# Optimization experiments

Measured on AMD Instinct MI355X. Metric: run time of the kernel, lower is better.

## Reference

```python
import jax, jax.numpy as jnp
import numpy as np

NUM_GROUPS = 256   # number of distinct gt instance ids per image
EPS = 1e-6
PULL_W = 1.0
PUSH_W = 1.0
LOSS_W = 1.0


def setup_inputs() -> dict:
    key = jax.random.key(0)
    k1, k2, k3 = jax.random.split(key, 3)
    B, N, D = 16, 16384, 256
    pred = jax.random.normal(k1, (B, N, D), dtype=jnp.float32)
    gt_inds = jax.random.randint(k2, (B, N), 0, NUM_GROUPS, dtype=jnp.int32)
    anchor_inds = jax.random.randint(k3, (B, N), 0, 9, dtype=jnp.int32)
    return {"pred": pred, "gt_inds": gt_inds, "anchor_inds": anchor_inds}


def _single_image_loss(p, g):
    # p: [N, D] tag embeddings, g: [N] int group ids in [0, NUM_GROUPS)
    ones = jnp.ones(g.shape, dtype=p.dtype)
    counts = jax.ops.segment_sum(ones, g, num_segments=NUM_GROUPS)          # [G]
    sums = jax.ops.segment_sum(p, g, num_segments=NUM_GROUPS)               # [G, D]
    tags = sums / jnp.maximum(counts, 1.0)[:, None]                         # group means

    # pull: per-element cosine to own group's tag (torch cos eps clamp on norm product)
    tag_per = tags[g]                                                       # [N, D]
    dot = jnp.sum(p * tag_per, axis=1)
    denom = jnp.maximum(jnp.linalg.norm(p, axis=1) * jnp.linalg.norm(tag_per, axis=1), EPS)
    one_minus_cos = 1.0 - dot / denom                                       # [N]
    pull_g = jax.ops.segment_sum(one_minus_cos, g, num_segments=NUM_GROUPS) / jnp.maximum(counts, 1.0)

    present = counts > 0
    obj_num = jnp.sum(present.astype(p.dtype))
    pull = jnp.sum(jnp.where(present, pull_g, 0.0)) / (obj_num + EPS)

    # push: pairwise cosine over group tags (incl. diagonal, then subtract 2*obj_num)
    tn = jnp.linalg.norm(tags, axis=1)                                      # [G]
    cosmat = (tags @ tags.T) / jnp.maximum(tn[:, None] * tn[None, :], EPS)  # [G, G]
    pair_mask = present[:, None] & present[None, :]
    push_sum = jnp.sum(jnp.where(pair_mask, 1.0 + cosmat, 0.0)) - 2.0 * obj_num
    push = push_sum / (((obj_num - 1.0) * obj_num + EPS) * 2.0)

    loss = PUSH_W * push + PULL_W * pull
    # original returns 0 when only a single group exists
    return jnp.where(obj_num > 1.0, loss, 0.0)


def reference(pred, gt_inds, anchor_inds):
    per_img = jax.vmap(_single_image_loss)(pred, gt_inds)   # [B]
    return LOSS_W * jnp.mean(per_img)
```

## Files before the change

### kernel.cpp

```cpp
#include <hip/hip_runtime.h>

#define B_ 16
#define N_ 16384
#define D_ 256
#define G_ 256
#define EPSF 1e-6f

template <int CTRL>
__device__ __forceinline__ float dpp_add_step(float x) {
    const int y = __builtin_amdgcn_update_dpp(0, __float_as_int(x), CTRL, 0xF, 0xF, false);
    return x + __int_as_float(y);
}
__device__ __forceinline__ float wave_sum64(float x) {
    x = dpp_add_step<0x111>(x);
    x = dpp_add_step<0x112>(x);
    x = dpp_add_step<0x114>(x);
    x = dpp_add_step<0x118>(x);
    x = dpp_add_step<0x142>(x);
    x = dpp_add_step<0x143>(x);
    return __int_as_float(__builtin_amdgcn_readlane(__float_as_int(x), 63));
}

__global__ __launch_bounds__(1024) void k_sort(const int* __restrict__ gt,
                                               int* __restrict__ counts,
                                               int* __restrict__ starts,
                                               int* __restrict__ sorted,
                                               int* __restrict__ done) {
    __shared__ int hist[G_];
    __shared__ int scn[G_];
    const int tid = threadIdx.x, b = blockIdx.x;
    if (b == 0 && tid == 0) done[0] = 0;
    if (tid < G_) hist[tid] = 0;
    __syncthreads();
    const int base = b * N_;
    #pragma unroll
    for (int k = 0; k < N_/4096; ++k) {
        const int4 g4 = *(const int4*)&gt[base + k*4096 + tid*4];
        atomicAdd(&hist[g4.x], 1);
        atomicAdd(&hist[g4.y], 1);
        atomicAdd(&hist[g4.z], 1);
        atomicAdd(&hist[g4.w], 1);
    }
    __syncthreads();
    int c = 0;
    if (tid < G_) {
        c = hist[tid];
        counts[b*G_ + tid] = c;
        scn[tid] = c;
    }
    __syncthreads();
    for (int off = 1; off < G_; off <<= 1) {
        int v = 0;
        if (tid < G_ && tid >= off) v = scn[tid - off];
        __syncthreads();
        if (tid < G_) scn[tid] += v;
        __syncthreads();
    }
    if (tid < G_) {
        const int st = scn[tid] - c;
        starts[b*G_ + tid] = st;
        hist[tid] = st;
    }
    __syncthreads();
    #pragma unroll
    for (int k = 0; k < N_/4096; ++k) {
        const int r = k*4096 + tid*4;
        const int4 g4 = *(const int4*)&gt[base + r];
        sorted[base + atomicAdd(&hist[g4.x], 1)] = r;
        sorted[base + atomicAdd(&hist[g4.y], 1)] = r + 1;
        sorted[base + atomicAdd(&hist[g4.z], 1)] = r + 2;
        sorted[base + atomicAdd(&hist[g4.w], 1)] = r + 3;
    }
}

__global__ __launch_bounds__(256, 5) void k_fused(const float* __restrict__ pred,
                                                  const int* __restrict__ sorted,
                                                  const int* __restrict__ starts,
                                                  const int* __restrict__ counts,
                                                  float* __restrict__ sums,
                                                  float* __restrict__ pull_g) {
    __shared__ float comb[2][2][2][D_];
    const int tid = threadIdx.x, lane = tid & 63, w = tid >> 6;
    const int sub = w >> 1, h = w & 1;
    const int gi = (blockIdx.x << 1) | sub;
    const int b = gi >> 8;
    const int start = starts[gi], cnt = counts[gi];
    const int c = lane * 4;

    const float* predb = pred + (size_t)b*N_*D_;
    const int*   sortb = sorted + b*N_ + start;

    float4 acc  = make_float4(0.f,0.f,0.f,0.f);
    float4 uacc = make_float4(0.f,0.f,0.f,0.f);

    const int half = (cnt + 1) >> 1;
    const int lo = h * half;
    const int hi = min(cnt, lo + half);
    int i = lo;

    if (cnt > 0 && cnt <= 128) {
        const int ids0 = sortb[min(lane, cnt-1)];
        int ids1 = 0;
        if (cnt > 64) ids1 = sortb[min(64 + lane, cnt-1)];
        #define GET2(k) (((k) < 64) ? __builtin_amdgcn_readlane(ids0, (k)) \
                                    : __builtin_amdgcn_readlane(ids1, (k) - 64))
        for (; i + 8 <= hi; i += 8) {
            const int r0 = GET2(i+0), r1 = GET2(i+1), r2 = GET2(i+2), r3 = GET2(i+3);
            const int r4 = GET2(i+4), r5 = GET2(i+5), r6 = GET2(i+6), r7 = GET2(i+7);
            const float4 p0 = *(const float4*)&predb[(size_t)r0*D_ + c];
            const float4 p1 = *(const float4*)&predb[(size_t)r1*D_ + c];
            const float4 p2 = *(const float4*)&predb[(size_t)r2*D_ + c];
            const float4 p3 = *(const float4*)&predb[(size_t)r3*D_ + c];
            const float4 p4 = *(const float4*)&predb[(size_t)r4*D_ + c];
            const float4 p5 = *(const float4*)&predb[(size_t)r5*D_ + c];
            const float4 p6 = *(const float4*)&predb[(size_t)r6*D_ + c];
            const float4 p7 = *(const float4*)&predb[(size_t)r7*D_ + c];
            float n0 = p0.x*p0.x + p0.y*p0.y + p0.z*p0.z + p0.w*p0.w;
            float n1 = p1.x*p1.x + p1.y*p1.y + p1.z*p1.z + p1.w*p1.w;
            float n2 = p2.x*p2.x + p2.y*p2.y + p2.z*p2.z + p2.w*p2.w;
            float n3 = p3.x*p3.x + p3.y*p3.y + p3.z*p3.z + p3.w*p3.w;
            float n4 = p4.x*p4.x + p4.y*p4.y + p4.z*p4.z + p4.w*p4.w;
            float n5 = p5.x*p5.x + p5.y*p5.y + p5.z*p5.z + p5.w*p5.w;
            float n6 = p6.x*p6.x + p6.y*p6.y + p6.z*p6.z + p6.w*p6.w;
            float n7 = p7.x*p7.x + p7.y*p7.y + p7.z*p7.z + p7.w*p7.w;
            n0 = wave_sum64(n0); n1 = wave_sum64(n1);
            n2 = wave_sum64(n2); n3 = wave_sum64(n3);
            n4 = wave_sum64(n4); n5 = wave_sum64(n5);
            n6 = wave_sum64(n6); n7 = wave_sum64(n7);
            const float q0 = __frsqrt_rn(n0), q1 = __frsqrt_rn(n1);
            const float q2 = __frsqrt_rn(n2), q3 = __frsqrt_rn(n3);
            const float q4 = __frsqrt_rn(n4), q5 = __frsqrt_rn(n5);
            const float q6 = __frsqrt_rn(n6), q7 = __frsqrt_rn(n7);
            acc.x  += ((p0.x + p1.x) + (p2.x + p3.x)) + ((p4.x + p5.x) + (p6.x + p7.x));
            acc.y  += ((p0.y + p1.y) + (p2.y + p3.y)) + ((p4.y + p5.y) + (p6.y + p7.y));
            acc.z  += ((p0.z + p1.z) + (p2.z + p3.z)) + ((p4.z + p5.z) + (p6.z + p7.z));
            acc.w  += ((p0.w + p1.w) + (p2.w + p3.w)) + ((p4.w + p5.w) + (p6.w + p7.w));
            uacc.x += ((p0.x*q0 + p1.x*q1) + (p2.x*q2 + p3.x*q3)) + ((p4.x*q4 + p5.x*q5) + (p6.x*q6 + p7.x*q7));
            uacc.y += ((p0.y*q0 + p1.y*q1) + (p2.y*q2 + p3.y*q3)) + ((p4.y*q4 + p5.y*q5) + (p6.y*q6 + p7.y*q7));
            uacc.z += ((p0.z*q0 + p1.z*q1) + (p2.z*q2 + p3.z*q3)) + ((p4.z*q4 + p5.z*q5) + (p6.z*q6 + p7.z*q7));
            uacc.w += ((p0.w*q0 + p1.w*q1) + (p2.w*q2 + p3.w*q3)) + ((p4.w*q4 + p5.w*q5) + (p6.w*q6 + p7.w*q7));
        }
        for (; i < hi; ++i) {
            const int r0 = GET2(i);
            const float4 p0 = *(const float4*)&predb[(size_t)r0*D_ + c];
            const float n0 = wave_sum64(p0.x*p0.x + p0.y*p0.y + p0.z*p0.z + p0.w*p0.w);
            const float q0 = __frsqrt_rn(n0);
            acc.x  += p0.x;    acc.y  += p0.y;    acc.z  += p0.z;    acc.w  += p0.w;
            uacc.x += p0.x*q0; uacc.y += p0.y*q0; uacc.z += p0.z*q0; uacc.w += p0.w*q0;
        }
        #undef GET2
    } else if (cnt > 128) {
        for (; i < hi; ++i) {
            const int r0 = sortb[i];
            const float4 p0 = *(const float4*)&predb[(size_t)r0*D_ + c];
            const float n0 = wave_sum64(p0.x*p0.x + p0.y*p0.y + p0.z*p0.z + p0.w*p0.w);
            const float q0 = __frsqrt_rn(n0);
            acc.x  += p0.x;    acc.y  += p0.y;    acc.z  += p0.z;    acc.w  += p0.w;
            uacc.x += p0.x*q0; uacc.y += p0.y*q0; uacc.z += p0.z*q0; uacc.w += p0.w*q0;
        }
    }

    *(float4*)&comb[sub][h][0][c] = acc;
    *(float4*)&comb[sub][h][1][c] = uacc;
    __syncthreads();
    if (h != 0) return;

    const float4 a2 = *(const float4*)&comb[sub][1][0][c];
    const float4 u2 = *(const float4*)&comb[sub][1][1][c];
    acc.x  += a2.x;  acc.y  += a2.y;  acc.z  += a2.z;  acc.w  += a2.w;
    uacc.x += u2.x;  uacc.y += u2.y;  uacc.z += u2.z;  uacc.w += u2.w;

    *(float4*)&sums[(size_t)gi*D_ + c] = acc;
    if (cnt == 0) {
        if (lane == 0) pull_g[gi] = 0.f;
        return;
    }
    const float ssq = wave_sum64(acc.x*acc.x + acc.y*acc.y + acc.z*acc.z + acc.w*acc.w);
    const float dus = wave_sum64(uacc.x*acc.x + uacc.y*acc.y + uacc.z*acc.z + uacc.w*acc.w);
    if (lane == 0) pull_g[gi] = (float)cnt - dus / sqrtf(ssq);
}

__global__ __launch_bounds__(256) void k_tags(const float* __restrict__ sums,
                                              const int* __restrict__ counts,
                                              const float* __restrict__ pull_g,
                                              float* __restrict__ lossv,
                                              int* __restrict__ done,
                                              float* __restrict__ out) {
    const int b = blockIdx.x;
    const int tid = threadIdx.x;
    const int lane = tid & 63;
    const int wave = tid >> 6;
    __shared__ float s_acc[D_];
    __shared__ float redA[256];
    __shared__ float redB[256];

    for (int i = tid; i < D_; i += 256) s_acc[i] = 0.f;
    __syncthreads();

    const int c = lane * 4;
    float4 sl = make_float4(0.f, 0.f, 0.f, 0.f);
    for (int g = wave; g < G_; g += 4) {
        const int cnt = counts[b*G_ + g];
        const float inv = 1.0f / fmaxf((float)cnt, 1.0f);
        const float4 sm = *(const float4*)&sums[((size_t)(b*G_ + g))*D_ + c];
        const float tx = sm.x*inv, tyv = sm.y*inv, tz = sm.z*inv, tw = sm.w*inv;
        const float sq = wave_sum64(tx*tx + tyv*tyv + tz*tz + tw*tw);
        if (cnt > 0) {
            const float it = __frsqrt_rn(sq);
            sl.x += tx*it; sl.y += tyv*it; sl.z += tz*it; sl.w += tw*it;
        }
    }
    atomicAdd(&s_acc[c+0], sl.x);
    atomicAdd(&s_acc[c+1], sl.y);
    atomicAdd(&s_acc[c+2], sl.z);
    atomicAdd(&s_acc[c+3], sl.w);
    __syncthreads();

    const int cnt_t = counts[b*G_ + tid];
    const float v = s_acc[tid];
    redA[tid] = v * v;
    redB[tid] = (cnt_t > 0) ? 1.f : 0.f;
    __syncthreads();
    for (int s = 128; s > 0; s >>= 1) {
        if (tid < s) { redA[tid] += redA[tid + s]; redB[tid] += redB[tid + s]; }
        __syncthreads();
    }
    float ssq = 0.f, obj = 0.f;
    if (tid == 0) { ssq = redA[0]; obj = redB[0]; }
    __syncthreads();

    redA[tid] = (cnt_t > 0) ? pull_g[b*G_ + tid] / (float)cnt_t : 0.f;
    __syncthreads();
    for (int s = 128; s > 0; s >>= 1) {
        if (tid < s) redA[tid] += redA[tid + s];
        __syncthreads();
    }
    if (tid == 0) {
        const float push = (obj*obj - 2.f*obj + ssq) / (((obj - 1.f)*obj + EPSF) * 2.f);
        const float pull = redA[0] / (obj + EPSF);
        const float loss = (obj > 1.f) ? (push + pull) : 0.f;
        __hip_atomic_store(&lossv[b], loss, __ATOMIC_RELEASE, __HIP_MEMORY_SCOPE_AGENT);
        const int o = __hip_atomic_fetch_add(&done[0], 1, __ATOMIC_ACQ_REL,
                                             __HIP_MEMORY_SCOPE_AGENT);
        if (o == B_ - 1) {
            float t = 0.f;
            #pragma unroll
            for (int bb = 0; bb < B_; ++bb)
                t += __hip_atomic_load(&lossv[bb], __ATOMIC_RELAXED, __HIP_MEMORY_SCOPE_AGENT);
            out[0] = t * (1.0f / (float)B_);
        }
    }
}

extern "C" void kernel_launch(void* const* d_in, const int* in_sizes, int n_in,
                              void* d_out, int out_size, void* d_ws, size_t ws_size,
                              hipStream_t stream) {
    const float* pred = (const float*)d_in[0];
    const int*   gt   = (const int*)d_in[1];
    float* out = (float*)d_out;

    char* ws = (char*)d_ws;
    const size_t SZ_SUMS = (size_t)B_*G_*D_*sizeof(float);
    const size_t SZ_I    = (size_t)B_*G_*sizeof(int);

    float* sums    = (float*)ws;                               ws += SZ_SUMS;
    int*   counts  = (int*)ws;                                 ws += SZ_I;
    int*   starts  = (int*)ws;                                 ws += SZ_I;
    float* pull_g  = (float*)ws;                               ws += SZ_I;
    float* lossv   = (float*)ws;                               ws += 64*sizeof(float);
    int*   done    = (int*)ws;                                 ws += 64*sizeof(int);
    int*   sorted  = (int*)ws;

    k_sort  <<<B_,      1024, 0, stream>>>(gt, counts, starts, sorted, done);
    k_fused <<<B_*G_/2,  256, 0, stream>>>(pred, sorted, starts, counts, sums, pull_g);
    k_tags  <<<B_,       256, 0, stream>>>(sums, counts, pull_g, lossv, done, out);
}
```

Measured before the change: 90.74 us.

## Split per-image counting sort into chunked histogram and scatter kernels

Replaces the single-block-per-image counting sort (16 blocks) with two kernels over 256 blocks: a per-chunk histogram, then a kernel that computes per-chunk prefix offsets and the global scan and scatters indices. The aim is to spread the sort across more CUs instead of 16. In exchange it adds an extra kernel launch, a global round trip for the chunk histograms, and redundant scans in every block.

```diff
diff --git a/kernel.cpp b/kernel.cpp
--- a/kernel.cpp
+++ b/kernel.cpp
@@ -5,6 +5,8 @@
 #define D_ 256
 #define G_ 256
 #define EPSF 1e-6f
+#define CHUNKS 16
+#define CROWS (N_/CHUNKS)
 
 template <int CTRL>
 __device__ __forceinline__ float dpp_add_step(float x) {
@@ -21,56 +23,61 @@
     return __int_as_float(__builtin_amdgcn_readlane(__float_as_int(x), 63));
 }
 
-__global__ __launch_bounds__(1024) void k_sort(const int* __restrict__ gt,
-                                               int* __restrict__ counts,
-                                               int* __restrict__ starts,
-                                               int* __restrict__ sorted,
-                                               int* __restrict__ done) {
-    __shared__ int hist[G_];
+__global__ __launch_bounds__(256) void k_hist(const int* __restrict__ gt,
+                                              int* __restrict__ chist,
+                                              int* __restrict__ done) {
+    __shared__ int h[G_];
+    const int tid = threadIdx.x, blk = blockIdx.x;
+    if (blk == 0 && tid == 0) done[0] = 0;
+    h[tid] = 0;
+    __syncthreads();
+    const int4 g4 = *(const int4*)&gt[blk*CROWS + tid*4];
+    atomicAdd(&h[g4.x], 1);
+    atomicAdd(&h[g4.y], 1);
+    atomicAdd(&h[g4.z], 1);
+    atomicAdd(&h[g4.w], 1);
+    __syncthreads();
+    chist[blk*G_ + tid] = h[tid];
+}
+
+__global__ __launch_bounds__(256) void k_scatscan(const int* __restrict__ gt,
+                                                  const int* __restrict__ chist,
+                                                  int* __restrict__ counts,
+                                                  int* __restrict__ starts,
+                                                  int* __restrict__ sorted) {
     __shared__ int scn[G_];
-    const int tid = threadIdx.x, b = blockIdx.x;
-    if (b == 0 && tid == 0) done[0] = 0;
-    if (tid < G_) hist[tid] = 0;
-    __syncthreads();
-    const int base = b * N_;
+    __shared__ int cur[G_];
+    const int g = threadIdx.x, blk = blockIdx.x;
+    const int b = blk >> 4, chunk = blk & 15;
+
+    int tot = 0, pre = 0;
     #pragma unroll
-    for (int k = 0; k < N_/4096; ++k) {
-        const int4 g4 = *(const int4*)&gt[base + k*4096 + tid*4];
-        atomicAdd(&hist[g4.x], 1);
-        atomicAdd(&hist[g4.y], 1);
-        atomicAdd(&hist[g4.z], 1);
-        atomicAdd(&hist[g4.w], 1);
-    }
-    __syncthreads();
-    int c = 0;
-    if (tid < G_) {
-        c = hist[tid];
-        counts[b*G_ + tid] = c;
-        scn[tid] = c;
-    }
+    for (int cc = 0; cc < CHUNKS; ++cc) {
+        const int v = chist[((b<<4) + cc)*G_ + g];
+        pre += (cc < chunk) ? v : 0;
+        tot += v;
+    }
+    scn[g] = tot;
     __syncthreads();
     for (int off = 1; off < G_; off <<= 1) {
-        int v = 0;
-        if (tid < G_ && tid >= off) v = scn[tid - off];
-        __syncthreads();
-        if (tid < G_) scn[tid] += v;
-        __syncthreads();
-    }
-    if (tid < G_) {
-        const int st = scn[tid] - c;
-        starts[b*G_ + tid] = st;
-        hist[tid] = st;
-    }
-    __syncthreads();
-    #pragma unroll
-    for (int k = 0; k < N_/4096; ++k) {
-        const int r = k*4096 + tid*4;
-        const int4 g4 = *(const int4*)&gt[base + r];
-        sorted[base + atomicAdd(&hist[g4.x], 1)] = r;
-        sorted[base + atomicAdd(&hist[g4.y], 1)] = r + 1;
-        sorted[base + atomicAdd(&hist[g4.z], 1)] = r + 2;
-        sorted[base + atomicAdd(&hist[g4.w], 1)] = r + 3;
-    }
+        const int v2 = (g >= off) ? scn[g - off] : 0;
+        __syncthreads();
+        scn[g] += v2;
+        __syncthreads();
+    }
+    const int st = scn[g] - tot;
+    if (chunk == 0) { counts[b*G_ + g] = tot; starts[b*G_ + g] = st; }
+    cur[g] = st + pre;
+    __syncthreads();
+
+    const int rbase = chunk * CROWS;
+    const int4 g4 = *(const int4*)&gt[b*N_ + rbase + g*4];
+    const int r = rbase + g*4;
+    int* sb = sorted + b*N_;
+    sb[atomicAdd(&cur[g4.x], 1)] = r;
+    sb[atomicAdd(&cur[g4.y], 1)] = r + 1;
+    sb[atomicAdd(&cur[g4.z], 1)] = r + 2;
+    sb[atomicAdd(&cur[g4.w], 1)] = r + 3;
 }
 
 __global__ __launch_bounds__(256, 5) void k_fused(const float* __restrict__ pred,
@@ -269,9 +276,11 @@
     float* pull_g  = (float*)ws;                               ws += SZ_I;
     float* lossv   = (float*)ws;                               ws += 64*sizeof(float);
     int*   done    = (int*)ws;                                 ws += 64*sizeof(int);
-    int*   sorted  = (int*)ws;
-
-    k_sort  <<<B_,      1024, 0, stream>>>(gt, counts, starts, sorted, done);
-    k_fused <<<B_*G_/2,  256, 0, stream>>>(pred, sorted, starts, counts, sums, pull_g);
-    k_tags  <<<B_,       256, 0, stream>>>(sums, counts, pull_g, lossv, done, out);
-}
+    int*   sorted  = (int*)ws;                                 ws += (size_t)B_*N_*sizeof(int);
+    int*   chist   = (int*)ws;
+
+    k_hist     <<<B_*CHUNKS, 256, 0, stream>>>(gt, chist, done);
+    k_scatscan <<<B_*CHUNKS, 256, 0, stream>>>(gt, chist, counts, starts, sorted);
+    k_fused    <<<B_*G_/2,   256, 0, stream>>>(pred, sorted, starts, counts, sums, pull_g);
+    k_tags     <<<B_,        256, 0, stream>>>(sums, counts, pull_g, lossv, done, out);
+}
```

Measured after the change: 85.44 us. 5.8% less time.
